# Kernel tuning notes

Measured on AMD Instinct MI355X. Metric: run time of the kernel, lower is better.

## Reference

```python
import jax, jax.numpy as jnp
import numpy as np

BS, NUM_VISIT, MAX_FEAT, MAX_TARGET = 32, 6, 12, 16
NUM_FEAT, NUM_REL, HIDDEN, REDUCED, OUT = 1992, 11, 128, 256, 90
GAMMA = 0.1


def setup_inputs() -> dict:
    key = jax.random.key(0)
    ks = jax.random.split(key, 20)
    u = lambda k, shape: jax.random.uniform(k, shape, dtype=jnp.float32)
    # one/multi-hot-like dense float inputs (per docstring)
    feat_index = (u(ks[0], (BS, NUM_VISIT, MAX_FEAT, NUM_FEAT)) < 0.01).astype(jnp.float32)
    neighbor_index = (u(ks[1], (BS, NUM_VISIT, MAX_FEAT, MAX_TARGET, NUM_FEAT)) < 0.001).astype(jnp.float32)
    rel_index = (u(ks[2], (BS, NUM_VISIT, MAX_FEAT, MAX_TARGET, NUM_REL)) < 0.2).astype(jnp.float32)
    # parameters (torch.rand init in the original; xavier for embedding)
    bound = float(np.sqrt(6.0 / (NUM_FEAT + HIDDEN)))
    emb_weight = jax.random.uniform(ks[3], (NUM_FEAT, HIDDEN), dtype=jnp.float32, minval=-bound, maxval=bound)
    return {
        "feat_index": feat_index,
        "neighbor_index": neighbor_index,
        "rel_index": rel_index,
        "emb_weight": emb_weight,
        "W_edge": u(ks[4], (NUM_REL, HIDDEN)),
        "W_v": u(ks[5], (REDUCED, HIDDEN)),
        "W_r": u(ks[6], (REDUCED, HIDDEN)),
        "b_v": u(ks[7], (REDUCED,)),
        "b_r": u(ks[8], (REDUCED,)),
        "W_alpha": u(ks[9], (NUM_FEAT,)),
        "b_alpha": u(ks[10], (MAX_FEAT,)),
        "W_beta": u(ks[11], (MAX_FEAT,)),
        "b_beta": u(ks[12], (NUM_VISIT,)),
        "W_l": u(ks[13], (REDUCED, REDUCED)),
        "b_l": u(ks[14], (REDUCED,)),
        "fc_W": u(ks[15], (OUT, 2 * REDUCED)) * 0.05,
        "fc_b": u(ks[16], (OUT,)) * 0.05,
    }


def reference(feat_index, neighbor_index, rel_index, emb_weight, W_edge, W_v, W_r,
              b_v, b_r, W_alpha, b_alpha, W_beta, b_beta, W_l, b_l, fc_W, fc_b):
    num_visit = feat_index.shape[1]
    # decay buffer lamb[i] = exp(-gamma*(num_visit - i))
    lamb = jnp.exp(-GAMMA * (num_visit - jnp.arange(num_visit, dtype=feat_index.dtype)))

    # node-level attention alpha: (b,v,m)
    alpha = jax.nn.softmax(jnp.einsum('n,bvmn->bvm', W_alpha, feat_index) + b_alpha)
    # visit-level attention beta: (b,v), modulated by temporal decay
    beta = jnp.tanh(jnp.einsum('m,bvm->bv', W_beta, alpha) + b_beta) * lamb

    # reduced node embeddings: (num_feat, reduced)
    reduced_emb = emb_weight @ W_v.T + b_v
    # attention-weighted neighbor aggregation; sum over targets t fused in
    attn = alpha * beta[:, :, None]                       # (b,v,m)
    node_agg = jnp.einsum('bvm,bvmtn,nr->bvmr', attn, neighbor_index, reduced_emb)

    # reduced edge (relation) embeddings: (num_rel, reduced)
    reduced_edge = W_edge @ W_r.T + b_r
    edge_agg = jnp.einsum('bvmtr,rd->bvmd', rel_index, reduced_edge)  # sum over t fused

    agg = node_agg + edge_agg                             # (b,v,m,reduced)
    # einsum('dd, bvfd -> bvfd') in torch takes the diagonal of W_l
    h = jax.nn.relu(jnp.diagonal(W_l) * agg + b_l)        # (b,v,m,reduced)

    h_g = h.sum(axis=(1, 2))                              # (b, reduced)
    # einsum('bvmn,bvmr->bvnr').sum(n).sum(v) == contract over v,m,n
    h_p = jnp.einsum('bvm,bvmr->br', feat_index.sum(-1), h)

    z_joint = jnp.concatenate([h_g, h_p], axis=-1)        # (b, 2*reduced)
    return jax.nn.sigmoid(z_joint @ fc_W.T + fc_b)
```

## Files before the change

kernel.cpp:

```cpp
#include <hip/hip_runtime.h>
#include <math.h>

#define BS   32
#define NV   6
#define MF   12
#define MT   16
#define NF   1992
#define NR   11
#define HID  128
#define RED  256
#define OUTD 90
#define GAMMA 0.1f

typedef float f4_t __attribute__((ext_vector_type(4)));

#define WS_HG    0
#define WS_HP    (WS_HG + BS*RED)
#define WS_ATTN  (WS_HP + BS*RED)
#define WS_FSUM  (WS_ATTN + BS*NV*MF)
#define WS_REMB  (WS_FSUM + BS*NV*MF)
#define WS_REDGE (WS_REMB + NF*RED)
#define WS_WTV   (WS_REDGE + NR*RED)
#define WS_WTR   (WS_WTV + HID*RED)
#define WS_FCWT  (WS_WTR + HID*RED)

#define N_ZERO (2*BS*RED)
#define N_WTV  (HID*RED)
#define N_WTR  (HID*RED)
#define N_FCWT (2*RED*OUTD)
#define PREP_ELEMS (N_ZERO + N_WTV + N_WTR + N_FCWT)
#define PREP_BLOCKS (PREP_ELEMS / 256)

__global__ __launch_bounds__(256) void k_prep_attn(
        const float* __restrict__ W_v, const float* __restrict__ W_r,
        const float* __restrict__ fc_W,
        const float* __restrict__ feat, const float* __restrict__ W_alpha,
        const float* __restrict__ b_alpha, const float* __restrict__ W_beta,
        const float* __restrict__ b_beta,
        float* __restrict__ ws_base,
        float* __restrict__ WT_v, float* __restrict__ WT_r, float* __restrict__ fcWT,
        float* __restrict__ attn_ws, float* __restrict__ fsum_ws) {
    int blk = blockIdx.x;
    int tid = threadIdx.x;
    if (blk < PREP_BLOCKS) {
        int i = blk * 256 + tid;
        if (i < N_ZERO) {
            ws_base[i] = 0.f;
        } else if (i < N_ZERO + N_WTV) {
            int j = i - N_ZERO;
            int k = j >> 8, r = j & 255;
            WT_v[j] = W_v[r * HID + k];
        } else if (i < N_ZERO + N_WTV + N_WTR) {
            int j = i - (N_ZERO + N_WTV);
            int k = j >> 8, r = j & 255;
            WT_r[j] = W_r[r * HID + k];
        } else {
            int j = i - (N_ZERO + N_WTV + N_WTR);
            int jj = j / OUTD, o = j - jj * OUTD;
            fcWT[j] = fc_W[o * (2 * RED) + jj];
        }
        return;
    }
    int bv   = blk - PREP_BLOCKS;
    int v    = bv % NV;
    int wave = tid >> 6;
    int lane = tid & 63;
    __shared__ float dot12[MF], fs12[MF];
    const float* base = feat + (size_t)bv * MF * NF;
    for (int m = wave; m < MF; m += 4) {
        const float4* rw = (const float4*)(base + (size_t)m * NF);
        const float4* wa = (const float4*)W_alpha;
        float da = 0.f, fs = 0.f;
        for (int i = lane; i < NF / 4; i += 64) {
            float4 x = rw[i];
            float4 w = wa[i];
            da += w.x * x.x + w.y * x.y + w.z * x.z + w.w * x.w;
            fs += x.x + x.y + x.z + x.w;
        }
        #pragma unroll
        for (int off = 32; off > 0; off >>= 1) {
            da += __shfl_xor(da, off);
            fs += __shfl_xor(fs, off);
        }
        if (lane == 0) { dot12[m] = da; fs12[m] = fs; }
    }
    __syncthreads();
    if (tid == 0) {
        float logits[MF];
        float mx = -1e30f;
        for (int m = 0; m < MF; ++m) { logits[m] = dot12[m] + b_alpha[m]; mx = fmaxf(mx, logits[m]); }
        float s = 0.f;
        for (int m = 0; m < MF; ++m) { logits[m] = expf(logits[m] - mx); s += logits[m]; }
        float inv = 1.f / s;
        float bdot = 0.f;
        for (int m = 0; m < MF; ++m) { logits[m] *= inv; bdot += W_beta[m] * logits[m]; }
        float lamb = expf(-GAMMA * (float)(NV - v));
        float beta = tanhf(bdot + b_beta[v]) * lamb;
        for (int m = 0; m < MF; ++m) {
            attn_ws[bv * MF + m] = logits[m] * beta;
            fsum_ws[bv * MF + m] = fs12[m];
        }
    }
}

#define NPB 8
#define NODE_BLOCKS (NF / NPB)
__global__ __launch_bounds__(256) void k_reduce(
        const float* __restrict__ emb, const float* __restrict__ W_edge,
        const float* __restrict__ WT_v, const float* __restrict__ WT_r,
        const float* __restrict__ b_v, const float* __restrict__ b_r,
        float* __restrict__ remb, float* __restrict__ redge) {
    int blk = blockIdx.x;
    int tid = threadIdx.x;
    if (blk < NODE_BLOCKS) {
        __shared__ float rows[NPB][HID];
        int n0 = blk * NPB;
        for (int i = tid; i < NPB * HID; i += 256)
            rows[i >> 7][i & 127] = emb[(size_t)n0 * HID + i];
        __syncthreads();
        float bv0 = b_v[tid];
        float a0 = bv0, a1 = bv0, a2 = bv0, a3 = bv0;
        float a4 = bv0, a5 = bv0, a6 = bv0, a7 = bv0;
        #pragma unroll 4
        for (int k = 0; k < HID; ++k) {
            float w = WT_v[k * RED + tid];
            a0 += rows[0][k] * w;
            a1 += rows[1][k] * w;
            a2 += rows[2][k] * w;
            a3 += rows[3][k] * w;
            a4 += rows[4][k] * w;
            a5 += rows[5][k] * w;
            a6 += rows[6][k] * w;
            a7 += rows[7][k] * w;
        }
        float* dst = remb + (size_t)n0 * RED + tid;
        dst[0*RED] = a0; dst[1*RED] = a1; dst[2*RED] = a2; dst[3*RED] = a3;
        dst[4*RED] = a4; dst[5*RED] = a5; dst[6*RED] = a6; dst[7*RED] = a7;
    } else {
        int e = blk - NODE_BLOCKS;
        __shared__ float row[HID];
        if (tid < HID) row[tid] = W_edge[e * HID + tid];
        __syncthreads();
        float acc = b_r[tid];
        #pragma unroll 4
        for (int k = 0; k < HID; ++k)
            acc += row[k] * WT_r[k * RED + tid];
        redge[e * RED + tid] = acc;
    }
}

#define NZCAP 1024
__global__ __launch_bounds__(256) void k_agg(
        const float* __restrict__ nbr, const float* __restrict__ rel,
        const float* __restrict__ remb, const float* __restrict__ redge,
        const float* __restrict__ attn_ws, const float* __restrict__ fsum_ws,
        const float* __restrict__ W_l, const float* __restrict__ b_l,
        float* __restrict__ h_g, float* __restrict__ h_p) {
    int bvm = blockIdx.x;
    int b   = bvm / (NV * MF);
    int tid = threadIdx.x;
    __shared__ int   nz_n[NZCAP];
    __shared__ float nz_v[NZCAP];
    __shared__ float rsum[NR];
    __shared__ int   cnt;
    if (tid == 0) cnt = 0;

    const f4_t* base = (const f4_t*)(nbr + (size_t)bvm * MT * NF);
    f4_t a0 = (f4_t)(0.f);
    f4_t a1 = (f4_t)(0.f);
    const bool has1 = (tid + 256) < (NF / 4);
    #pragma unroll 4
    for (int t = 0; t < MT; ++t) {
        const f4_t* r4 = base + t * (NF / 4);
        f4_t x = __builtin_nontemporal_load(r4 + tid);
        a0 += x;
        if (has1) {
            f4_t y = __builtin_nontemporal_load(r4 + tid + 256);
            a1 += y;
        }
    }

    if (tid < NR) {
        const float* rb = rel + (size_t)bvm * MT * NR;
        float s = 0.f;
        #pragma unroll
        for (int t = 0; t < MT; ++t) s += rb[t * NR + tid];
        rsum[tid] = s;
    }
    __syncthreads();

    {
        int nb = tid * 4;
        #pragma unroll
        for (int c = 0; c < 4; ++c)
            if (a0[c] != 0.f) {
                int p = atomicAdd(&cnt, 1);
                if (p < NZCAP) { nz_n[p] = nb + c; nz_v[p] = a0[c]; }
            }
        if (has1) {
            nb = (tid + 256) * 4;
            #pragma unroll
            for (int c = 0; c < 4; ++c)
                if (a1[c] != 0.f) {
                    int p = atomicAdd(&cnt, 1);
                    if (p < NZCAP) { nz_n[p] = nb + c; nz_v[p] = a1[c]; }
                }
        }
    }
    __syncthreads();

    int r = tid;
    int c = min(cnt, NZCAP);
    float node = 0.f;
    for (int i = 0; i < c; ++i)
        node += nz_v[i] * remb[(size_t)nz_n[i] * RED + r];
    float edge = 0.f;
    #pragma unroll
    for (int j = 0; j < NR; ++j)
        edge += rsum[j] * redge[j * RED + r];
    float a  = attn_ws[bvm];
    float fs = fsum_ws[bvm];
    float agg = a * node + edge;
    float h = fmaxf(0.f, W_l[(size_t)r * RED + r] * agg + b_l[r]);
    atomicAdd(&h_g[b * RED + r], h);
    atomicAdd(&h_p[b * RED + r], fs * h);
}

__global__ __launch_bounds__(256) void k_out(
        const float* __restrict__ h_g, const float* __restrict__ h_p,
        const float* __restrict__ fcWT, const float* __restrict__ fc_b,
        float* __restrict__ out) {
    int b   = blockIdx.x;
    int tid = threadIdx.x;
    __shared__ float z[2 * RED];
    __shared__ float part[2][OUTD];
    for (int j = tid; j < RED; j += 256) {
        z[j]       = h_g[b * RED + j];
        z[RED + j] = h_p[b * RED + j];
    }
    __syncthreads();
    int o = tid & 127, half = tid >> 7;
    if (o < OUTD) {
        float acc = 0.f;
        int j0 = half * RED;
        #pragma unroll 8
        for (int j = j0; j < j0 + RED; ++j)
            acc += z[j] * fcWT[j * OUTD + o];
        part[half][o] = acc;
    }
    __syncthreads();
    if (tid < OUTD) {
        float acc = part[0][tid] + part[1][tid] + fc_b[tid];
        out[b * OUTD + tid] = 1.f / (1.f + expf(-acc));
    }
}

extern "C" void kernel_launch(void* const* d_in, const int* in_sizes, int n_in,
                              void* d_out, int out_size, void* d_ws, size_t ws_size,
                              hipStream_t stream) {
    const float* feat    = (const float*)d_in[0];
    const float* nbr     = (const float*)d_in[1];
    const float* rel     = (const float*)d_in[2];
    const float* emb     = (const float*)d_in[3];
    const float* W_edge  = (const float*)d_in[4];
    const float* W_v     = (const float*)d_in[5];
    const float* W_r     = (const float*)d_in[6];
    const float* b_v     = (const float*)d_in[7];
    const float* b_r     = (const float*)d_in[8];
    const float* W_alpha = (const float*)d_in[9];
    const float* b_alpha = (const float*)d_in[10];
    const float* W_beta  = (const float*)d_in[11];
    const float* b_beta  = (const float*)d_in[12];
    const float* W_l     = (const float*)d_in[13];
    const float* b_l     = (const float*)d_in[14];
    const float* fc_W    = (const float*)d_in[15];
    const float* fc_b    = (const float*)d_in[16];

    float* ws    = (float*)d_ws;
    float* hg    = ws + WS_HG;
    float* hp    = ws + WS_HP;
    float* attn  = ws + WS_ATTN;
    float* fsum  = ws + WS_FSUM;
    float* remb  = ws + WS_REMB;
    float* redge = ws + WS_REDGE;
    float* WT_v  = ws + WS_WTV;
    float* WT_r  = ws + WS_WTR;
    float* fcWT  = ws + WS_FCWT;

    k_prep_attn<<<PREP_BLOCKS + BS * NV, 256, 0, stream>>>(
        W_v, W_r, fc_W, feat, W_alpha, b_alpha, W_beta, b_beta,
        ws, WT_v, WT_r, fcWT, attn, fsum);
    k_reduce<<<NODE_BLOCKS + NR, 256, 0, stream>>>(
        emb, W_edge, WT_v, WT_r, b_v, b_r, remb, redge);
    k_agg<<<BS * NV * MF, 256, 0, stream>>>(
        nbr, rel, remb, redge, attn, fsum, W_l, b_l, hg, hp);
    k_out<<<BS, 256, 0, stream>>>(hg, hp, fcWT, fc_b, (float*)d_out);
}
```

Before: 454.5 us.

## Move neighbor streaming and sparse compaction into the first kernel, ahead of embedding reduction

```diff
diff --git a/kernel.cpp b/kernel.cpp
--- a/kernel.cpp
+++ b/kernel.cpp
@@ -11,6 +11,7 @@
 #define RED  256
 #define OUTD 90
 #define GAMMA 0.1f
+#define NZCAP 1024
 
 typedef float f4_t __attribute__((ext_vector_type(4)));
 
@@ -23,25 +24,88 @@
 #define WS_WTV   (WS_REDGE + NR*RED)
 #define WS_WTR   (WS_WTV + HID*RED)
 #define WS_FCWT  (WS_WTR + HID*RED)
-
+#define WS_DIAG  (WS_FCWT + 2*RED*OUTD)
+#define WS_CNT   (WS_DIAG + RED)
+#define WS_RSUM  (WS_CNT + BS*NV*MF)
+#define WS_NZN   (WS_RSUM + BS*NV*MF*NR)
+#define WS_NZV   (WS_NZN + BS*NV*MF*NZCAP)
+
+#define STREAM_BLOCKS (BS*NV*MF)
 #define N_ZERO (2*BS*RED)
 #define N_WTV  (HID*RED)
 #define N_WTR  (HID*RED)
 #define N_FCWT (2*RED*OUTD)
-#define PREP_ELEMS (N_ZERO + N_WTV + N_WTR + N_FCWT)
+#define N_DIAG RED
+#define PREP_ELEMS (N_ZERO + N_WTV + N_WTR + N_FCWT + N_DIAG)
 #define PREP_BLOCKS (PREP_ELEMS / 256)
 
-__global__ __launch_bounds__(256) void k_prep_attn(
+__global__ __launch_bounds__(256) void k_stream_prep_attn(
+        const float* __restrict__ nbr, const float* __restrict__ rel,
         const float* __restrict__ W_v, const float* __restrict__ W_r,
-        const float* __restrict__ fc_W,
+        const float* __restrict__ fc_W, const float* __restrict__ W_l,
         const float* __restrict__ feat, const float* __restrict__ W_alpha,
         const float* __restrict__ b_alpha, const float* __restrict__ W_beta,
         const float* __restrict__ b_beta,
         float* __restrict__ ws_base,
         float* __restrict__ WT_v, float* __restrict__ WT_r, float* __restrict__ fcWT,
+        float* __restrict__ diag,
+        int* __restrict__ cnt_g, float* __restrict__ rsum_g,
+        int* __restrict__ nzn_g, float* __restrict__ nzv_g,
         float* __restrict__ attn_ws, float* __restrict__ fsum_ws) {
     int blk = blockIdx.x;
     int tid = threadIdx.x;
+
+    if (blk < STREAM_BLOCKS) {
+        int bvm = blk;
+        __shared__ int   nz_n[NZCAP];
+        __shared__ float nz_v[NZCAP];
+        __shared__ int   cnt;
+        if (tid == 0) cnt = 0;
+        const f4_t* base = (const f4_t*)(nbr + (size_t)bvm * MT * NF);
+        f4_t a0 = (f4_t)(0.f);
+        f4_t a1 = (f4_t)(0.f);
+        const bool has1 = (tid + 256) < (NF / 4);
+        #pragma unroll 4
+        for (int t = 0; t < MT; ++t) {
+            const f4_t* r4 = base + t * (NF / 4);
+            a0 += __builtin_nontemporal_load(r4 + tid);
+            if (has1) a1 += __builtin_nontemporal_load(r4 + tid + 256);
+        }
+        float rs = 0.f;
+        if (tid < NR) {
+            const float* rb = rel + (size_t)bvm * MT * NR;
+            #pragma unroll
+            for (int t = 0; t < MT; ++t) rs += rb[t * NR + tid];
+        }
+        __syncthreads();
+        int nb = tid * 4;
+        #pragma unroll
+        for (int c = 0; c < 4; ++c)
+            if (a0[c] != 0.f) {
+                int p = atomicAdd(&cnt, 1);
+                if (p < NZCAP) { nz_n[p] = nb + c; nz_v[p] = a0[c]; }
+            }
+        if (has1) {
+            nb = (tid + 256) * 4;
+            #pragma unroll
+            for (int c = 0; c < 4; ++c)
+                if (a1[c] != 0.f) {
+                    int p = atomicAdd(&cnt, 1);
+                    if (p < NZCAP) { nz_n[p] = nb + c; nz_v[p] = a1[c]; }
+                }
+        }
+        __syncthreads();
+        int c = min(cnt, NZCAP);
+        if (tid == 0) cnt_g[bvm] = c;
+        if (tid < NR) rsum_g[bvm * NR + tid] = rs;
+        for (int i = tid; i < c; i += 256) {
+            nzn_g[bvm * NZCAP + i] = nz_n[i];
+            nzv_g[bvm * NZCAP + i] = nz_v[i];
+        }
+        return;
+    }
+    blk -= STREAM_BLOCKS;
+
     if (blk < PREP_BLOCKS) {
         int i = blk * 256 + tid;
         if (i < N_ZERO) {
@@ -54,13 +118,17 @@
             int j = i - (N_ZERO + N_WTV);
             int k = j >> 8, r = j & 255;
             WT_r[j] = W_r[r * HID + k];
-        } else {
+        } else if (i < N_ZERO + N_WTV + N_WTR + N_FCWT) {
             int j = i - (N_ZERO + N_WTV + N_WTR);
             int jj = j / OUTD, o = j - jj * OUTD;
             fcWT[j] = fc_W[o * (2 * RED) + jj];
+        } else {
+            int j = i - (N_ZERO + N_WTV + N_WTR + N_FCWT);
+            diag[j] = W_l[(size_t)j * RED + j];
         }
         return;
     }
+
     int bv   = blk - PREP_BLOCKS;
     int v    = bv % NV;
     int wave = tid >> 6;
@@ -149,12 +217,12 @@
     }
 }
 
-#define NZCAP 1024
-__global__ __launch_bounds__(256) void k_agg(
-        const float* __restrict__ nbr, const float* __restrict__ rel,
+__global__ __launch_bounds__(256) void k_gather(
         const float* __restrict__ remb, const float* __restrict__ redge,
+        const int* __restrict__ cnt_g, const float* __restrict__ rsum_g,
+        const int* __restrict__ nzn_g, const float* __restrict__ nzv_g,
         const float* __restrict__ attn_ws, const float* __restrict__ fsum_ws,
-        const float* __restrict__ W_l, const float* __restrict__ b_l,
+        const float* __restrict__ diag, const float* __restrict__ b_l,
         float* __restrict__ h_g, float* __restrict__ h_p) {
     int bvm = blockIdx.x;
     int b   = bvm / (NV * MF);
@@ -162,55 +230,14 @@
     __shared__ int   nz_n[NZCAP];
     __shared__ float nz_v[NZCAP];
     __shared__ float rsum[NR];
-    __shared__ int   cnt;
-    if (tid == 0) cnt = 0;
-
-    const f4_t* base = (const f4_t*)(nbr + (size_t)bvm * MT * NF);
-    f4_t a0 = (f4_t)(0.f);
-    f4_t a1 = (f4_t)(0.f);
-    const bool has1 = (tid + 256) < (NF / 4);
-    #pragma unroll 4
-    for (int t = 0; t < MT; ++t) {
-        const f4_t* r4 = base + t * (NF / 4);
-        f4_t x = __builtin_nontemporal_load(r4 + tid);
-        a0 += x;
-        if (has1) {
-            f4_t y = __builtin_nontemporal_load(r4 + tid + 256);
-            a1 += y;
-        }
-    }
-
-    if (tid < NR) {
-        const float* rb = rel + (size_t)bvm * MT * NR;
-        float s = 0.f;
-        #pragma unroll
-        for (int t = 0; t < MT; ++t) s += rb[t * NR + tid];
-        rsum[tid] = s;
+    int c = cnt_g[bvm];
+    if (tid < NR) rsum[tid] = rsum_g[bvm * NR + tid];
+    for (int i = tid; i < c; i += 256) {
+        nz_n[i] = nzn_g[bvm * NZCAP + i];
+        nz_v[i] = nzv_g[bvm * NZCAP + i];
     }
     __syncthreads();
-
-    {
-        int nb = tid * 4;
-        #pragma unroll
-        for (int c = 0; c < 4; ++c)
-            if (a0[c] != 0.f) {
-                int p = atomicAdd(&cnt, 1);
-                if (p < NZCAP) { nz_n[p] = nb + c; nz_v[p] = a0[c]; }
-            }
-        if (has1) {
-            nb = (tid + 256) * 4;
-            #pragma unroll
-            for (int c = 0; c < 4; ++c)
-                if (a1[c] != 0.f) {
-                    int p = atomicAdd(&cnt, 1);
-                    if (p < NZCAP) { nz_n[p] = nb + c; nz_v[p] = a1[c]; }
-                }
-        }
-    }
-    __syncthreads();
-
     int r = tid;
-    int c = min(cnt, NZCAP);
     float node = 0.f;
     for (int i = 0; i < c; ++i)
         node += nz_v[i] * remb[(size_t)nz_n[i] * RED + r];
@@ -221,7 +248,7 @@
     float a  = attn_ws[bvm];
     float fs = fsum_ws[bvm];
     float agg = a * node + edge;
-    float h = fmaxf(0.f, W_l[(size_t)r * RED + r] * agg + b_l[r]);
+    float h = fmaxf(0.f, diag[r] * agg + b_l[r]);
     atomicAdd(&h_g[b * RED + r], h);
     atomicAdd(&h_p[b * RED + r], fs * h);
 }
@@ -286,13 +313,18 @@
     float* WT_v  = ws + WS_WTV;
     float* WT_r  = ws + WS_WTR;
     float* fcWT  = ws + WS_FCWT;
-
-    k_prep_attn<<<PREP_BLOCKS + BS * NV, 256, 0, stream>>>(
-        W_v, W_r, fc_W, feat, W_alpha, b_alpha, W_beta, b_beta,
-        ws, WT_v, WT_r, fcWT, attn, fsum);
+    float* diag  = ws + WS_DIAG;
+    int*   cnt_g = (int*)(ws + WS_CNT);
+    float* rsum_g= ws + WS_RSUM;
+    int*   nzn_g = (int*)(ws + WS_NZN);
+    float* nzv_g = ws + WS_NZV;
+
+    k_stream_prep_attn<<<STREAM_BLOCKS + PREP_BLOCKS + BS * NV, 256, 0, stream>>>(
+        nbr, rel, W_v, W_r, fc_W, W_l, feat, W_alpha, b_alpha, W_beta, b_beta,
+        ws, WT_v, WT_r, fcWT, diag, cnt_g, rsum_g, nzn_g, nzv_g, attn, fsum);
     k_reduce<<<NODE_BLOCKS + NR, 256, 0, stream>>>(
         emb, W_edge, WT_v, WT_r, b_v, b_r, remb, redge);
-    k_agg<<<BS * NV * MF, 256, 0, stream>>>(
-        nbr, rel, remb, redge, attn, fsum, W_l, b_l, hg, hp);
+    k_gather<<<BS * NV * MF, 256, 0, stream>>>(
+        remb, redge, cnt_g, rsum_g, nzn_g, nzv_g, attn, fsum, diag, b_l, hg, hp);
     k_out<<<BS, 256, 0, stream>>>(hg, hp, fcWT, fc_b, (float*)d_out);
 }
```

New measurement: 449.1 us (median of 2 runs). About the same (-1.2%).
